# Performance work log

Measured on AMD Instinct MI355X. Metric: run time of the kernel, lower is better.

## Reference

```python
import jax, jax.numpy as jnp
import numpy as np

# Sizes: seq_len S, batch B, nodes N, embed D, candidates K, depth L (emb_depth=6)
S, B, N, D, K, L = 8, 16, 500, 128, 50, 6


def setup_inputs() -> dict:
    key = jax.random.key(0)
    ks = jax.random.split(key, 8)
    x = jax.random.uniform(ks[0], (S, B, N, 2), dtype=jnp.float32)  # TSP coords in [0,1)^2
    def w(k, shape, fan):
        return jax.random.normal(k, shape, dtype=jnp.float32) * (1.0 / np.sqrt(fan))
    Wn = w(ks[1], (2, D), 2)          # node (coord) encoder
    bn = jnp.zeros((D,), jnp.float32)
    Ws = w(ks[2], (L, D, D), D)       # per-layer self transform
    Wm = w(ks[3], (L, D, D), D)       # per-layer message transform
    bL = jnp.zeros((L, D), jnp.float32)
    we = jax.random.normal(ks[4], (L,), dtype=jnp.float32)  # per-layer edge-distance gate scale
    be = jnp.zeros((L,), jnp.float32)                        # per-layer edge-distance gate bias
    Wo = w(ks[5], (D, D), D)          # output projection after global mean pool
    return {"x": x, "Wn": Wn, "bn": bn, "Ws": Ws, "Wm": Wm, "bL": bL,
            "we": we, "be": be, "Wo": Wo}


def _forward(x, Wn, bn, Ws, Wm, bL, we, be, Wo):
    S_, B_, N_, F = x.shape
    G = S_ * B_
    coords = x.reshape(G, N_, F)                                  # (G,N,2)

    # --- candidate edge selection: per-node K nearest neighbors (cdist + top-k) ---
    diff = coords[:, :, None, :] - coords[:, None, :, :]          # (G,N,N,2)
    dist = jnp.sqrt(jnp.sum(diff * diff, axis=-1) + 1e-12)        # (G,N,N) euclidean cdist
    big = jnp.asarray(1e9, x.dtype)
    d_noself = dist + jnp.eye(N_, dtype=x.dtype) * big            # exclude self edges
    _, nn_idx = jax.lax.top_k(-d_noself, K)                       # (G,N,K) K smallest distances
    gi = jnp.arange(G)[:, None, None]
    ni = jnp.arange(N_)[None, :, None]
    A = jnp.zeros((G, N_, N_), x.dtype).at[gi, ni, nn_idx].set(1.0)
    A = jnp.maximum(A, jnp.swapaxes(A, 1, 2))                     # undirected, deduped edge set

    # --- GNN (Net: emb_depth=6 SiLU message-passing, distance-gated edges) ---
    h = jax.nn.silu(coords @ Wn + bn)                             # (G,N,D)
    for l in range(L):
        gate = jax.nn.silu(we[l] * dist + be[l]) * A              # (G,N,N) edge weights on kNN graph
        m = jnp.einsum('gij,gjd->gid', gate, h)                   # neighbor aggregation
        h = jax.nn.silu(h @ Ws[l] + m @ Wm[l] + bL[l])
    graph = jnp.mean(h, axis=1) @ Wo                              # global_mean_pool + proj (G,D)
    return graph.reshape(S_, B_, -1)                              # (S,B,D) node_embeddings


def reference(x, Wn, bn, Ws, Wm, bL, we, be, Wo):
    return _forward(x, Wn, bn, Ws, Wm, bL, we, be, Wo)
```

## Files before the change

### kernel.cpp

```cpp
#include <hip/hip_runtime.h>
#include <hip/hip_bf16.h>
#include <stdint.h>

#define G_   128
#define N_   500
#define NP_  512
#define D_   128
#define K_   50
#define L_   6
#define NW_  16
#define ROWT 125

typedef __attribute__((ext_vector_type(8))) short bf16x8;
typedef __attribute__((ext_vector_type(4))) float f32x4;

#define ADJ_BYTES  ((size_t)G_ * N_ * NW_ * 4)
#define ADJS_BYTES ((size_t)G_ * NP_ * NW_ * 4)
#define HB_BYTES   ((size_t)G_ * NP_ * D_ * 2)
#define WT_BYTES   ((size_t)L_ * D_ * D_ * 2)

#define L_C2 0
#define L_AM 4096
#define L_B0 12288
#define L_B1 45056
#define LDS_TOTAL 77824

__device__ __forceinline__ float silu_f(float z) {
    return z * __builtin_amdgcn_rcpf(1.0f + __expf(-z));
}
__device__ __forceinline__ unsigned short f2bf(float f) {
    uint32_t u = __float_as_uint(f);
    u += 0x7fffu + ((u >> 16) & 1u);
    return (unsigned short)(u >> 16);
}
__device__ __forceinline__ float bf2f(unsigned short s) {
    return __uint_as_float(((uint32_t)s) << 16);
}

__global__ __launch_bounds__(256) void knn_kernel(const float* __restrict__ x,
                                                  uint32_t* __restrict__ adj) {
    int g    = blockIdx.x / ROWT;
    int tile = blockIdx.x % ROWT;
    int wv   = threadIdx.x >> 6;
    int lane = threadIdx.x & 63;
    int i    = tile * 4 + wv;

    __shared__ float2 c[N_];
    for (int t = threadIdx.x; t < N_; t += 256)
        c[t] = ((const float2*)x)[(size_t)g * N_ + t];
    __syncthreads();

    float2 ci = c[i];
    uint32_t kb[8];
#pragma unroll
    for (int r = 0; r < 8; ++r) {
        int j = lane + r * 64;
        float dv;
        if (j < N_ && j != i) {
            float dx = ci.x - c[j].x, dy = ci.y - c[j].y;
            dv = dx * dx + dy * dy;
        } else {
            dv = 3.0e38f;
        }
        kb[r] = __float_as_uint(dv);
    }

    uint32_t prefix = 0;
    for (int bit = 29; bit >= 0; --bit) {
        uint32_t cand = prefix | (1u << bit);
        int cnt = 0;
#pragma unroll
        for (int r = 0; r < 8; ++r)
            cnt += __popcll(__ballot(kb[r] < cand));
        if (cnt < K_) prefix = cand;
    }

    unsigned long long sel[8];
    int cntless = 0;
#pragma unroll
    for (int r = 0; r < 8; ++r) {
        sel[r] = __ballot(kb[r] < prefix);
        cntless += __popcll(sel[r]);
    }
    int rem = K_ - cntless;
    unsigned long long tb[8];
    int tietot = 0;
#pragma unroll
    for (int r = 0; r < 8; ++r) {
        tb[r] = __ballot(kb[r] == prefix);
        tietot += __popcll(tb[r]);
    }
    if (tietot == rem) {
#pragma unroll
        for (int r = 0; r < 8; ++r) sel[r] |= tb[r];
    } else {
#pragma unroll
        for (int r = 0; r < 8; ++r) {
            unsigned long long t2 = tb[r];
            while (rem > 0 && t2) {
                unsigned long long lb = t2 & (~t2 + 1ull);
                sel[r] |= lb;
                t2 ^= lb;
                --rem;
            }
        }
    }

    uint32_t* arow = adj + ((size_t)g * N_ + i) * NW_;
#pragma unroll
    for (int r = 0; r < 8; ++r) {
        if (lane == 2 * r)     arow[2 * r]     = (uint32_t)sel[r];
        if (lane == 2 * r + 1) arow[2 * r + 1] = (uint32_t)(sel[r] >> 32);
    }
}

__global__ __launch_bounds__(512) void sym_kernel(const uint32_t* __restrict__ adj,
                                                  uint32_t* __restrict__ adjS) {
    int g = blockIdx.x, tid = threadIdx.x;
    __shared__ uint32_t am[N_][NW_];
    const uint32_t* ag = adj + (size_t)g * N_ * NW_;
    for (int t = tid; t < N_ * NW_; t += 512) ((uint32_t*)am)[t] = ag[t];
    __syncthreads();
    uint32_t* og = adjS + (size_t)g * NP_ * NW_;
    for (int idx = tid; idx < N_ * NW_; idx += 512) {
        int ii = idx >> 4, w = idx & 15;
        uint32_t v = am[ii][w];
        int jb = w << 5;
        int jmax = (jb + 32 <= N_) ? 32 : (N_ - jb);
        uint32_t wi = (uint32_t)ii >> 5, bi = ii & 31;
        for (int b = 0; b < jmax; ++b)
            v |= ((am[jb + b][wi] >> bi) & 1u) << b;
        og[ii * NW_ + w] = v;
    }
    for (int idx = N_ * NW_ + tid; idx < NP_ * NW_; idx += 512)
        og[idx] = 0;
}

__global__ __launch_bounds__(256) void wprep_kernel(const float* __restrict__ Ws,
                                                    const float* __restrict__ Wm,
                                                    unsigned short* __restrict__ WsT,
                                                    unsigned short* __restrict__ WmT) {
    int idx = blockIdx.x * 256 + threadIdx.x;
    int half = idx >= L_ * D_ * D_;
    int r = half ? idx - L_ * D_ * D_ : idx;
    int l = r >> 14, rr = r & 16383, dout = rr >> 7, din = rr & 127;
    const float* W = half ? Wm : Ws;
    unsigned short* O = half ? WmT : WsT;
    O[r] = f2bf(W[(size_t)l * 16384 + din * 128 + dout]);
}

__global__ __launch_bounds__(256) void enc_kernel(const float* __restrict__ x,
                                                  const float* __restrict__ Wn,
                                                  const float* __restrict__ bn,
                                                  unsigned short* __restrict__ h,
                                                  unsigned short* __restrict__ hT) {
    int g = blockIdx.x, tid = threadIdx.x;
    __shared__ float2 c[N_];
    for (int t = tid; t < N_; t += 256)
        c[t] = ((const float2*)x)[(size_t)g * N_ + t];
    __syncthreads();
    for (int o = tid; o < N_ * 16; o += 256) {
        int i = o >> 4, d0 = (o & 15) * 8;
        float2 ci = c[i];
        unsigned short u[8];
#pragma unroll
        for (int e = 0; e < 8; ++e) {
            int d = d0 + e;
            u[e] = f2bf(silu_f(ci.x * Wn[d] + ci.y * Wn[D_ + d] + bn[d]));
        }
        *(uint4*)&h[((size_t)g * NP_ + i) * D_ + d0] = *(uint4*)u;
    }
    for (int o = tid; o < D_ * 64; o += 256) {
        int d = o >> 6, io = o & 63;
        float w0 = Wn[d], w1 = Wn[D_ + d], b = bn[d];
        unsigned short u[8];
#pragma unroll
        for (int e = 0; e < 8; ++e) {
            int i = io * 8 + e;
            unsigned short val = 0;
            if (i < N_) {
                float2 ci = c[i];
                val = f2bf(silu_f(ci.x * w0 + ci.y * w1 + b));
            }
            u[e] = val;
        }
        *(uint4*)&hT[((size_t)g * D_ + d) * NP_ + io * 8] = *(uint4*)u;
    }
}

__global__ __launch_bounds__(512, 4) void layer_kernel(
    const uint32_t* __restrict__ adjS,
    const float* __restrict__ x,
    const unsigned short* __restrict__ hin,
    const unsigned short* __restrict__ hinT,
    unsigned short* __restrict__ hout,
    unsigned short* __restrict__ houtT,
    const unsigned short* __restrict__ WsT,
    const unsigned short* __restrict__ WmT,
    const float* __restrict__ bL,
    const float* __restrict__ we,
    const float* __restrict__ be, int l)
{
    int bid = (blockIdx.x & 7) * 64 + (blockIdx.x >> 3);
    int g  = bid >> 2;
    int it = bid & 3;
    int i0 = it * 128;
    int tid = threadIdx.x;
    int lane = tid & 63, wv = tid >> 6;
    int wrow = wv >> 2, wcol = wv & 3;

    extern __shared__ char lds[];
    float2*   c2 = (float2*)(lds + L_C2);
    uint32_t* am = (uint32_t*)(lds + L_AM);
    char*     tileI = lds;
    char*     tileT = lds + 34816;

    for (int t = tid; t < N_; t += 512)
        c2[t] = ((const float2*)x)[(size_t)g * N_ + t];
    const uint32_t* aS = adjS + ((size_t)g * NP_ + i0) * NW_;
    for (int t = tid; t < 128 * NW_; t += 512) am[t] = aS[t];
    __syncthreads();

    float wel = we[l], bel = be[l];
    const unsigned short* hTg = hinT + (size_t)g * D_ * NP_;

    auto stage = [&](char* buf, int jt) {
        int j0t = jt * 64;
        char* hTA   = buf;
        char* gateB = buf + 16384;
        uint4 hv[2];
#pragma unroll
        for (int p = 0; p < 2; ++p) {
            int o = tid + p * 512;
            int d = o >> 3, jo = o & 7;
            hv[p] = *(const uint4*)&hTg[(size_t)d * NP_ + j0t + jo * 8];
        }
#pragma unroll
        for (int p = 0; p < 2; ++p) {
            int o = tid + p * 512;
            int il = o >> 3, jo = o & 7;
            int jb = j0t + jo * 8;
            uint32_t wbits = am[il * NW_ + (jb >> 5)];
            uint32_t b8 = (wbits >> (jb & 31)) & 0xffu;
            float2 ci = c2[i0 + il];
            unsigned short u[8];
#pragma unroll
            for (int e = 0; e < 8; ++e) {
                float2 cj = c2[jb + e];
                float dx = ci.x - cj.x, dy = ci.y - cj.y;
                float dist = __builtin_amdgcn_sqrtf(dx * dx + dy * dy + 1e-12f);
                float z = wel * dist + bel;
                float s = z * __builtin_amdgcn_rcpf(1.0f + __expf(-z));
                u[e] = ((b8 >> e) & 1u) ? f2bf(s) : (unsigned short)0;
            }
            int byt = (il << 7) + (jo << 4); byt ^= (il & 7) << 4;
            *(uint4*)(gateB + byt) = *(uint4*)u;
        }
#pragma unroll
        for (int p = 0; p < 2; ++p) {
            int o = tid + p * 512;
            int d = o >> 3, jo = o & 7;
            int byt = (d << 7) + (jo << 4); byt ^= (d & 7) << 4;
            *(uint4*)(hTA + byt) = hv[p];
        }
    };

    f32x4 acc[4][2];
#pragma unroll
    for (int a_ = 0; a_ < 4; ++a_)
#pragma unroll
        for (int b_ = 0; b_ < 2; ++b_)
            acc[a_][b_] = (f32x4){0.f, 0.f, 0.f, 0.f};

    stage(lds + L_B0, 0);
    __syncthreads();
    for (int jt = 0; jt < 8; ++jt) {
        char* cur = lds + ((jt & 1) ? L_B1 : L_B0);
        if (jt < 7) stage(lds + ((jt & 1) ? L_B0 : L_B1), jt + 1);
        char* hTA = cur, *gateB = cur + 16384;
#pragma unroll
        for (int kk = 0; kk < 64; kk += 32) {
            int kbyte = (kk + ((lane >> 4) << 3)) << 1;
            bf16x8 af[4], bfr[2];
#pragma unroll
            for (int fr = 0; fr < 4; ++fr) {
                int d = wrow * 64 + fr * 16 + (lane & 15);
                int byt = (d << 7) + kbyte; byt ^= (d & 7) << 4;
                af[fr] = *(const bf16x8*)(hTA + byt);
            }
#pragma unroll
            for (int fc = 0; fc < 2; ++fc) {
                int i = wcol * 32 + fc * 16 + (lane & 15);
                int byt = (i << 7) + kbyte; byt ^= (i & 7) << 4;
                bfr[fc] = *(const bf16x8*)(gateB + byt);
            }
#pragma unroll
            for (int fr = 0; fr < 4; ++fr)
#pragma unroll
                for (int fc = 0; fc < 2; ++fc)
                    acc[fr][fc] = __builtin_amdgcn_mfma_f32_16x16x32_bf16(
                        af[fr], bfr[fc], acc[fr][fc], 0, 0, 0);
        }
        __syncthreads();
    }

    char* Bt = lds + L_B1;
    char* At = lds + L_B0;
#pragma unroll
    for (int fr = 0; fr < 4; ++fr)
#pragma unroll
        for (int fc = 0; fc < 2; ++fc) {
            int dbase = wrow * 64 + fr * 16 + ((lane >> 4) << 2);
            int ib    = wcol * 32 + fc * 16 + (lane & 15);
            f32x4 v = acc[fr][fc];
            uint32_t p0 = (uint32_t)f2bf(v[0]) | ((uint32_t)f2bf(v[1]) << 16);
            uint32_t p1 = (uint32_t)f2bf(v[2]) | ((uint32_t)f2bf(v[3]) << 16);
            int byt = (ib << 8) + (dbase << 1); byt ^= (ib & 7) << 4;
            *(uint32_t*)(Bt + byt)     = p0;
            *(uint32_t*)(Bt + byt + 4) = p1;
        }
    const unsigned short* wmp = WmT + (size_t)l * D_ * D_;
#pragma unroll
    for (int p = 0; p < 4; ++p) {
        int o = tid + p * 512;
        int dout = o >> 4, ko = o & 15;
        uint4 v = *(const uint4*)&wmp[dout * 128 + ko * 8];
        int byt = (dout << 8) + (ko << 4); byt ^= (dout & 7) << 4;
        *(uint4*)(At + byt) = v;
    }
    __syncthreads();

    f32x4 acc2[4][2];
#pragma unroll
    for (int a_ = 0; a_ < 4; ++a_)
#pragma unroll
        for (int b_ = 0; b_ < 2; ++b_)
            acc2[a_][b_] = (f32x4){0.f, 0.f, 0.f, 0.f};

    auto gemm128 = [&]() {
#pragma unroll
        for (int kk = 0; kk < 128; kk += 32) {
            int kbyte = (kk + ((lane >> 4) << 3)) << 1;
            bf16x8 af[4], bfr[2];
#pragma unroll
            for (int fr = 0; fr < 4; ++fr) {
                int d = wrow * 64 + fr * 16 + (lane & 15);
                int byt = (d << 8) + kbyte; byt ^= (d & 7) << 4;
                af[fr] = *(const bf16x8*)(At + byt);
            }
#pragma unroll
            for (int fc = 0; fc < 2; ++fc) {
                int i = wcol * 32 + fc * 16 + (lane & 15);
                int byt = (i << 8) + kbyte; byt ^= (i & 7) << 4;
                bfr[fc] = *(const bf16x8*)(Bt + byt);
            }
#pragma unroll
            for (int fr = 0; fr < 4; ++fr)
#pragma unroll
                for (int fc = 0; fc < 2; ++fc)
                    acc2[fr][fc] = __builtin_amdgcn_mfma_f32_16x16x32_bf16(
                        af[fr], bfr[fc], acc2[fr][fc], 0, 0, 0);
        }
    };
    gemm128();
    __syncthreads();

    const unsigned short* hg = hin + (size_t)g * NP_ * D_;
#pragma unroll
    for (int p = 0; p < 4; ++p) {
        int o = tid + p * 512;
        int il = o >> 4, ko = o & 15;
        int gi = i0 + il;
        uint4 v = make_uint4(0u, 0u, 0u, 0u);
        if (gi < N_) v = *(const uint4*)&hg[(size_t)gi * D_ + ko * 8];
        int byt = (il << 8) + (ko << 4); byt ^= (il & 7) << 4;
        *(uint4*)(Bt + byt) = v;
    }
    const unsigned short* wsp = WsT + (size_t)l * D_ * D_;
#pragma unroll
    for (int p = 0; p < 4; ++p) {
        int o = tid + p * 512;
        int dout = o >> 4, ko = o & 15;
        uint4 v = *(const uint4*)&wsp[dout * 128 + ko * 8];
        int byt = (dout << 8) + (ko << 4); byt ^= (dout & 7) << 4;
        *(uint4*)(At + byt) = v;
    }
    __syncthreads();
    gemm128();

    __syncthreads();
    const float* blp = bL + (size_t)l * D_;
#pragma unroll
    for (int fr = 0; fr < 4; ++fr)
#pragma unroll
        for (int fc = 0; fc < 2; ++fc) {
            int dbase = wrow * 64 + fr * 16 + ((lane >> 4) << 2);
            int ib = wcol * 32 + fc * 16 + (lane & 15);
            int gi = i0 + ib;
            f32x4 v = acc2[fr][fc];
            float4 bias = *(const float4*)&blp[dbase];
            float o0 = silu_f(v[0] + bias.x);
            float o1 = silu_f(v[1] + bias.y);
            float o2 = silu_f(v[2] + bias.z);
            float o3 = silu_f(v[3] + bias.w);
            if (gi >= N_) { o0 = 0.f; o1 = 0.f; o2 = 0.f; o3 = 0.f; }
            unsigned short b0 = f2bf(o0), b1 = f2bf(o1);
            unsigned short b2 = f2bf(o2), b3 = f2bf(o3);
            char* pI = tileI + ib * 272 + dbase * 2;
            *(uint32_t*)pI       = (uint32_t)b0 | ((uint32_t)b1 << 16);
            *(uint32_t*)(pI + 4) = (uint32_t)b2 | ((uint32_t)b3 << 16);
            *(unsigned short*)(tileT + (dbase    ) * 272 + ib * 2) = b0;
            *(unsigned short*)(tileT + (dbase + 1) * 272 + ib * 2) = b1;
            *(unsigned short*)(tileT + (dbase + 2) * 272 + ib * 2) = b2;
            *(unsigned short*)(tileT + (dbase + 3) * 272 + ib * 2) = b3;
        }
    __syncthreads();
    unsigned short* hgO  = hout  + (size_t)g * NP_ * D_;
    unsigned short* hgOT = houtT + (size_t)g * D_ * NP_;
#pragma unroll
    for (int p = 0; p < 4; ++p) {
        int o = tid + p * 512;
        int r = o >> 4, seg = o & 15;
        uint4 vI = *(const uint4*)(tileI + r * 272 + seg * 16);
        *(uint4*)&hgO[(size_t)(i0 + r) * D_ + seg * 8] = vI;
        uint4 vT = *(const uint4*)(tileT + r * 272 + seg * 16);
        *(uint4*)&hgOT[(size_t)r * NP_ + i0 + seg * 8] = vT;
    }
}

__global__ __launch_bounds__(256) void pool_kernel(const unsigned short* __restrict__ h,
                                                   const float* __restrict__ Wo,
                                                   float* __restrict__ out) {
    int g = blockIdx.x, tid = threadIdx.x;
    const unsigned short* hg = h + (size_t)g * NP_ * D_;
    float a8[8];
#pragma unroll
    for (int e = 0; e < 8; ++e) a8[e] = 0.f;
    int d0 = (tid & 15) * 8;
    for (int i = tid >> 4; i < N_; i += 16) {
        uint4 v = *(const uint4*)&hg[(size_t)i * D_ + d0];
        const unsigned short* pu = (const unsigned short*)&v;
#pragma unroll
        for (int e = 0; e < 8; ++e) a8[e] += bf2f(pu[e]);
    }
    __shared__ float red[16][D_];
#pragma unroll
    for (int e = 0; e < 8; ++e) red[tid >> 4][d0 + e] = a8[e];
    __syncthreads();
    __shared__ float pooled[D_];
    if (tid < D_) {
        float s = 0.f;
#pragma unroll
        for (int grp = 0; grp < 16; ++grp) s += red[grp][tid];
        pooled[tid] = s * (1.0f / (float)N_);
    }
    __syncthreads();
    if (tid < D_) {
        float accv = 0.f;
        for (int k = 0; k < D_; ++k) accv += pooled[k] * Wo[(size_t)k * D_ + tid];
        out[(size_t)g * D_ + tid] = accv;
    }
}

extern "C" void kernel_launch(void* const* d_in, const int* in_sizes, int n_in,
                              void* d_out, int out_size, void* d_ws, size_t ws_size,
                              hipStream_t stream) {
    (void)in_sizes; (void)n_in; (void)out_size; (void)ws_size;
    const float* x  = (const float*)d_in[0];
    const float* Wn = (const float*)d_in[1];
    const float* bn = (const float*)d_in[2];
    const float* Ws = (const float*)d_in[3];
    const float* Wm = (const float*)d_in[4];
    const float* bL = (const float*)d_in[5];
    const float* we = (const float*)d_in[6];
    const float* be = (const float*)d_in[7];
    const float* Wo = (const float*)d_in[8];
    float* out = (float*)d_out;

    char* w = (char*)d_ws;
    uint32_t*       adj  = (uint32_t*)w;        w += ADJ_BYTES;
    uint32_t*       adjS = (uint32_t*)w;        w += ADJS_BYTES;
    unsigned short* hA   = (unsigned short*)w;  w += HB_BYTES;
    unsigned short* hAT  = (unsigned short*)w;  w += HB_BYTES;
    unsigned short* hB   = (unsigned short*)w;  w += HB_BYTES;
    unsigned short* hBT  = (unsigned short*)w;  w += HB_BYTES;
    unsigned short* WsT  = (unsigned short*)w;  w += WT_BYTES;
    unsigned short* WmT  = (unsigned short*)w;  w += WT_BYTES;

    hipFuncSetAttribute((const void*)layer_kernel,
                        hipFuncAttributeMaxDynamicSharedMemorySize, LDS_TOTAL);

    knn_kernel<<<G_ * ROWT, 256, 0, stream>>>(x, adj);
    sym_kernel<<<G_, 512, 0, stream>>>(adj, adjS);
    wprep_kernel<<<(2 * L_ * D_ * D_) / 256, 256, 0, stream>>>(Ws, Wm, WsT, WmT);
    enc_kernel<<<G_, 256, 0, stream>>>(x, Wn, bn, hA, hAT);

    for (int l = 0; l < L_; ++l) {
        const unsigned short* hi  = (l & 1) ? hB  : hA;
        const unsigned short* hiT = (l & 1) ? hBT : hAT;
        unsigned short* ho  = (l & 1) ? hA  : hB;
        unsigned short* hoT = (l & 1) ? hAT : hBT;
        layer_kernel<<<G_ * 4, 512, LDS_TOTAL, stream>>>(adjS, x, hi, hiT, ho, hoT,
                                                         WsT, WmT, bL, we, be, l);
    }

    pool_kernel<<<G_, 256, 0, stream>>>(hA, Wo, out);
}
```

Before: 508.6 us.

## Replace dense adjacency gate evaluation with precomputed sparse bucketed edge lists

```diff
diff --git a/kernel.cpp b/kernel.cpp
--- a/kernel.cpp
+++ b/kernel.cpp
@@ -15,15 +15,15 @@
 typedef __attribute__((ext_vector_type(4))) float f32x4;
 
 #define ADJ_BYTES  ((size_t)G_ * N_ * NW_ * 4)
-#define ADJS_BYTES ((size_t)G_ * NP_ * NW_ * 4)
+#define EBUF_BYTES ((size_t)G_ * 32 * 1024 * 4)
+#define ECNT_BYTES ((size_t)G_ * 32 * 4)
 #define HB_BYTES   ((size_t)G_ * NP_ * D_ * 2)
 #define WT_BYTES   ((size_t)L_ * D_ * D_ * 2)
 
-#define L_C2 0
-#define L_AM 4096
-#define L_B0 12288
-#define L_B1 45056
-#define LDS_TOTAL 77824
+#define L_B0   0
+#define L_B1   32768
+#define L_ECNT 69632
+#define LDS_TOTAL 69664
 
 __device__ __forceinline__ float silu_f(float z) {
     return z * __builtin_amdgcn_rcpf(1.0f + __expf(-z));
@@ -66,13 +66,20 @@
     }
 
     uint32_t prefix = 0;
-    for (int bit = 29; bit >= 0; --bit) {
-        uint32_t cand = prefix | (1u << bit);
-        int cnt = 0;
-#pragma unroll
-        for (int r = 0; r < 8; ++r)
-            cnt += __popcll(__ballot(kb[r] < cand));
-        if (cnt < K_) prefix = cand;
+    for (int bit = 28; bit >= 0; bit -= 2) {
+        uint32_t c1 = prefix + (1u << bit);
+        uint32_t c2 = prefix + (2u << bit);
+        uint32_t c3 = prefix + (3u << bit);
+        int n1 = 0, n2 = 0, n3 = 0;
+#pragma unroll
+        for (int r = 0; r < 8; ++r) {
+            n1 += __popcll(__ballot(kb[r] < c1));
+            n2 += __popcll(__ballot(kb[r] < c2));
+            n3 += __popcll(__ballot(kb[r] < c3));
+        }
+        if (n3 < K_)      prefix = c3;
+        else if (n2 < K_) prefix = c2;
+        else if (n1 < K_) prefix = c1;
     }
 
     unsigned long long sel[8];
@@ -114,14 +121,25 @@
     }
 }
 
-__global__ __launch_bounds__(512) void sym_kernel(const uint32_t* __restrict__ adj,
-                                                  uint32_t* __restrict__ adjS) {
+__global__ __launch_bounds__(512) void ebuild_kernel(const float* __restrict__ x,
+                                                     const uint32_t* __restrict__ adj,
+                                                     uint32_t* __restrict__ ebuf,
+                                                     uint32_t* __restrict__ ecnt) {
     int g = blockIdx.x, tid = threadIdx.x;
     __shared__ uint32_t am[N_][NW_];
+    __shared__ float2   c[N_];
+    __shared__ uint32_t bcnt[32];
+
+    for (int t = tid; t < N_; t += 512)
+        c[t] = ((const float2*)x)[(size_t)g * N_ + t];
     const uint32_t* ag = adj + (size_t)g * N_ * NW_;
-    for (int t = tid; t < N_ * NW_; t += 512) ((uint32_t*)am)[t] = ag[t];
-    __syncthreads();
-    uint32_t* og = adjS + (size_t)g * NP_ * NW_;
+    for (int t = tid; t < N_ * NW_; t += 512)
+        ((uint32_t*)am)[t] = ag[t];
+    if (tid < 32) bcnt[tid] = 0;
+    __syncthreads();
+
+    uint32_t buf[16];
+    int cnt = 0;
     for (int idx = tid; idx < N_ * NW_; idx += 512) {
         int ii = idx >> 4, w = idx & 15;
         uint32_t v = am[ii][w];
@@ -130,10 +148,35 @@
         uint32_t wi = (uint32_t)ii >> 5, bi = ii & 31;
         for (int b = 0; b < jmax; ++b)
             v |= ((am[jb + b][wi] >> bi) & 1u) << b;
-        og[ii * NW_ + w] = v;
-    }
-    for (int idx = N_ * NW_ + tid; idx < NP_ * NW_; idx += 512)
-        og[idx] = 0;
+        buf[cnt++] = v;
+    }
+    __syncthreads();
+
+    uint32_t* eg = ebuf + ((size_t)g << 15);
+    cnt = 0;
+    for (int idx = tid; idx < N_ * NW_; idx += 512) {
+        int ii = idx >> 4, w = idx & 15;
+        uint32_t v = buf[cnt++];
+        if (!v) continue;
+        float2 ci = c[ii];
+        int il = ii & 127;
+        int bb = (ii >> 7) << 3;
+        while (v) {
+            int b = __ffs(v) - 1;
+            v &= v - 1;
+            int j = (w << 5) + b;
+            int bucket = bb + (j >> 6);
+            uint32_t slot = atomicAdd(&bcnt[bucket], 1u);
+            float dx = ci.x - c[j].x, dy = ci.y - c[j].y;
+            float dd = sqrtf(dx * dx + dy * dy + 1e-12f);
+            uint32_t rec = ((uint32_t)il << 25) | ((uint32_t)(j & 63) << 19)
+                         | (__float_as_uint(dd) >> 11);
+            if (slot < 1024u)
+                eg[(bucket << 10) + slot] = rec;
+        }
+    }
+    __syncthreads();
+    if (tid < 32) ecnt[(g << 5) + tid] = bcnt[tid] > 1024u ? 1024u : bcnt[tid];
 }
 
 __global__ __launch_bounds__(256) void wprep_kernel(const float* __restrict__ Ws,
@@ -189,8 +232,8 @@
 }
 
 __global__ __launch_bounds__(512, 4) void layer_kernel(
-    const uint32_t* __restrict__ adjS,
-    const float* __restrict__ x,
+    const uint32_t* __restrict__ ebuf,
+    const uint32_t* __restrict__ ecnt,
     const unsigned short* __restrict__ hin,
     const unsigned short* __restrict__ hinT,
     unsigned short* __restrict__ hout,
@@ -210,24 +253,27 @@
     int wrow = wv >> 2, wcol = wv & 3;
 
     extern __shared__ char lds[];
-    float2*   c2 = (float2*)(lds + L_C2);
-    uint32_t* am = (uint32_t*)(lds + L_AM);
-    char*     tileI = lds;
-    char*     tileT = lds + 34816;
-
-    for (int t = tid; t < N_; t += 512)
-        c2[t] = ((const float2*)x)[(size_t)g * N_ + t];
-    const uint32_t* aS = adjS + ((size_t)g * NP_ + i0) * NW_;
-    for (int t = tid; t < 128 * NW_; t += 512) am[t] = aS[t];
-    __syncthreads();
+    uint32_t* ecnt_s = (uint32_t*)(lds + L_ECNT);
+    char* tileI = lds;
+    char* tileT = lds + 34816;
+
+    if (tid < 8) ecnt_s[tid] = ecnt[(g << 5) + (it << 3) + tid];
 
     float wel = we[l], bel = be[l];
     const unsigned short* hTg = hinT + (size_t)g * D_ * NP_;
-
+    const uint32_t* ebg = ebuf + ((size_t)g << 15) + ((size_t)it << 13);
+
+    auto zerogate = [&](char* buf) {
+        char* gb = buf + 16384;
+        const uint4 z4 = make_uint4(0u, 0u, 0u, 0u);
+#pragma unroll
+        for (int p = 0; p < 2; ++p)
+            *(uint4*)(gb + (tid + p * 512) * 16) = z4;
+    };
     auto stage = [&](char* buf, int jt) {
-        int j0t = jt * 64;
         char* hTA   = buf;
         char* gateB = buf + 16384;
+        int j0t = jt * 64;
         uint4 hv[2];
 #pragma unroll
         for (int p = 0; p < 2; ++p) {
@@ -235,26 +281,18 @@
             int d = o >> 3, jo = o & 7;
             hv[p] = *(const uint4*)&hTg[(size_t)d * NP_ + j0t + jo * 8];
         }
-#pragma unroll
-        for (int p = 0; p < 2; ++p) {
-            int o = tid + p * 512;
-            int il = o >> 3, jo = o & 7;
-            int jb = j0t + jo * 8;
-            uint32_t wbits = am[il * NW_ + (jb >> 5)];
-            uint32_t b8 = (wbits >> (jb & 31)) & 0xffu;
-            float2 ci = c2[i0 + il];
-            unsigned short u[8];
-#pragma unroll
-            for (int e = 0; e < 8; ++e) {
-                float2 cj = c2[jb + e];
-                float dx = ci.x - cj.x, dy = ci.y - cj.y;
-                float dist = __builtin_amdgcn_sqrtf(dx * dx + dy * dy + 1e-12f);
-                float z = wel * dist + bel;
-                float s = z * __builtin_amdgcn_rcpf(1.0f + __expf(-z));
-                u[e] = ((b8 >> e) & 1u) ? f2bf(s) : (unsigned short)0;
-            }
-            int byt = (il << 7) + (jo << 4); byt ^= (il & 7) << 4;
-            *(uint4*)(gateB + byt) = *(uint4*)u;
+        int n = (int)ecnt_s[jt];
+        const uint32_t* eb = ebg + (jt << 10);
+        for (int e = tid; e < n; e += 512) {
+            uint32_t rec = eb[e];
+            int il = rec >> 25;
+            int jl = (rec >> 19) & 63;
+            float dist = __uint_as_float((rec & 0x7FFFFu) << 11);
+            float z = wel * dist + bel;
+            float s = z * __builtin_amdgcn_rcpf(1.0f + __expf(-z));
+            int byt = (il << 7) + (jl << 1);
+            byt ^= (il & 7) << 4;
+            *(unsigned short*)(gateB + byt) = f2bf(s);
         }
 #pragma unroll
         for (int p = 0; p < 2; ++p) {
@@ -272,8 +310,12 @@
         for (int b_ = 0; b_ < 2; ++b_)
             acc[a_][b_] = (f32x4){0.f, 0.f, 0.f, 0.f};
 
+    zerogate(lds + L_B0);
+    zerogate(lds + L_B1);
+    __syncthreads();
     stage(lds + L_B0, 0);
     __syncthreads();
+
     for (int jt = 0; jt < 8; ++jt) {
         char* cur = lds + ((jt & 1) ? L_B1 : L_B0);
         if (jt < 7) stage(lds + ((jt & 1) ? L_B0 : L_B1), jt + 1);
@@ -301,6 +343,8 @@
                     acc[fr][fc] = __builtin_amdgcn_mfma_f32_16x16x32_bf16(
                         af[fr], bfr[fc], acc[fr][fc], 0, 0, 0);
         }
+        __syncthreads();
+        if (jt < 6) zerogate(cur);
         __syncthreads();
     }
 
@@ -479,7 +523,8 @@
 
     char* w = (char*)d_ws;
     uint32_t*       adj  = (uint32_t*)w;        w += ADJ_BYTES;
-    uint32_t*       adjS = (uint32_t*)w;        w += ADJS_BYTES;
+    uint32_t*       ebuf = (uint32_t*)w;        w += EBUF_BYTES;
+    uint32_t*       ecnt = (uint32_t*)w;        w += ECNT_BYTES;
     unsigned short* hA   = (unsigned short*)w;  w += HB_BYTES;
     unsigned short* hAT  = (unsigned short*)w;  w += HB_BYTES;
     unsigned short* hB   = (unsigned short*)w;  w += HB_BYTES;
@@ -491,7 +536,7 @@
                         hipFuncAttributeMaxDynamicSharedMemorySize, LDS_TOTAL);
 
     knn_kernel<<<G_ * ROWT, 256, 0, stream>>>(x, adj);
-    sym_kernel<<<G_, 512, 0, stream>>>(adj, adjS);
+    ebuild_kernel<<<G_, 512, 0, stream>>>(x, adj, ebuf, ecnt);
     wprep_kernel<<<(2 * L_ * D_ * D_) / 256, 256, 0, stream>>>(Ws, Wm, WsT, WmT);
     enc_kernel<<<G_, 256, 0, stream>>>(x, Wn, bn, hA, hAT);
 
@@ -500,7 +545,7 @@
         const unsigned short* hiT = (l & 1) ? hBT : hAT;
         unsigned short* ho  = (l & 1) ? hA  : hB;
         unsigned short* hoT = (l & 1) ? hAT : hBT;
-        layer_kernel<<<G_ * 4, 512, LDS_TOTAL, stream>>>(adjS, x, hi, hiT, ho, hoT,
+        layer_kernel<<<G_ * 4, 512, LDS_TOTAL, stream>>>(ebuf, ecnt, hi, hiT, ho, hoT,
                                                          WsT, WmT, bL, we, be, l);
     }
 
```

Measured after the change: 483.6 us. -4.9%, faster.
